# Kernel optimization log

Hardware: AMD Instinct MI355X
Metric: run time of the kernel (lower is better)

## Reference

```python
import jax, jax.numpy as jnp
import numpy as np

D = 128   # node feature dim
C = 2     # classes
N = 50000 # nodes
E = 500000  # edges (before self-loops)
H1 = 2    # conv1 heads
NEG_SLOPE = 0.2
BN_EPS = 1e-5


def setup_inputs() -> dict:
    key = jax.random.key(0)
    ks = jax.random.split(key, 24)
    rn = lambda k, shape, s=0.05: jax.random.normal(k, shape, dtype=jnp.float32) * s
    inp = {
        'x': jax.random.normal(ks[0], (N, D), dtype=jnp.float32),
        'edge_index': jax.random.randint(ks[1], (2, E), 0, N, dtype=jnp.int64),
        # conv1: GATConv(D, D, heads=2, concat=True)
        'W1': rn(ks[2], (D, H1 * D)),
        'att_src1': rn(ks[3], (H1, D)),
        'att_dst1': rn(ks[4], (H1, D)),
        'bias1': jnp.zeros((H1 * D,), jnp.float32),
        # conv2: GATConv(2D, D, heads=1, concat=False)
        'W2': rn(ks[5], (2 * D, D)),
        'att_src2': rn(ks[6], (1, D)),
        'att_dst2': rn(ks[7], (1, D)),
        'bias2': jnp.zeros((D,), jnp.float32),
        # lin1 = MLP([3D, 96]) : Linear -> ReLU -> BatchNorm1d
        'Wl': rn(ks[8], (3 * D, 96)), 'bl': jnp.zeros((96,), jnp.float32),
        'gl': jnp.ones((96,), jnp.float32), 'betal': jnp.zeros((96,), jnp.float32),
        # mlp1 = MLP([96, 96, C]) : two (Linear -> ReLU -> BN) blocks
        'Wa': rn(ks[9], (96, 96)), 'ba': jnp.zeros((96,), jnp.float32),
        'ga': jnp.ones((96,), jnp.float32), 'betaa': jnp.zeros((96,), jnp.float32),
        'Wb': rn(ks[10], (96, C)), 'bb': jnp.zeros((C,), jnp.float32),
        'gb': jnp.ones((C,), jnp.float32), 'betab': jnp.zeros((C,), jnp.float32),
    }
    return inp


def gat_conv(x, src, dst, W, att_src, att_dst, bias, heads, out_dim, concat):
    # PyG GATConv: h = x W -> [N,H,F]; per-edge logit leakyrelu(a_s.h_src + a_d.h_dst);
    # segment softmax over edges grouped by destination; weighted scatter-sum.
    n = x.shape[0]
    h = (x @ W).reshape(n, heads, out_dim)
    a_src = jnp.einsum('nhd,hd->nh', h, att_src)  # [N,H]
    a_dst = jnp.einsum('nhd,hd->nh', h, att_dst)
    alpha = jax.nn.leaky_relu(a_src[src] + a_dst[dst], NEG_SLOPE)  # [Etot,H]
    m = jax.ops.segment_max(alpha, dst, num_segments=n)            # [N,H]
    e = jnp.exp(alpha - m[dst])
    s = jax.ops.segment_sum(e, dst, num_segments=n)
    w = e / (s[dst] + 1e-16)                                       # [Etot,H]
    out = jax.ops.segment_sum(h[src] * w[:, :, None], dst, num_segments=n)  # [N,H,F]
    out = out.reshape(n, heads * out_dim) if concat else out.mean(axis=1)
    return out + bias


def mlp_block(x, W, b, gamma, beta):
    # Linear -> ReLU -> BatchNorm1d (training-mode batch stats, biased var)
    y = jax.nn.relu(x @ W + b)
    mu = y.mean(axis=0)
    var = ((y - mu) ** 2).mean(axis=0)
    return gamma * (y - mu) / jnp.sqrt(var + BN_EPS) + beta


def reference(x, edge_index, W1, att_src1, att_dst1, bias1,
              W2, att_src2, att_dst2, bias2,
              Wl, bl, gl, betal, Wa, ba, ga, betaa, Wb, bb, gb, betab):
    n = x.shape[0]
    # PyG GATConv default add_self_loops=True
    loops = jnp.arange(n, dtype=edge_index.dtype)
    src = jnp.concatenate([edge_index[0], loops])
    dst = jnp.concatenate([edge_index[1], loops])
    x1 = gat_conv(x, src, dst, W1, att_src1, att_dst1, bias1, H1, D, True)    # [N,2D]
    x2 = gat_conv(x1, src, dst, W2, att_src2, att_dst2, bias2, 1, D, False)   # [N,D]
    h = jnp.concatenate([x1, x2], axis=1)                                      # [N,3D]
    h = mlp_block(h, Wl, bl, gl, betal)     # lin1
    h = mlp_block(h, Wa, ba, ga, betaa)     # mlp1 layer 1
    h = mlp_block(h, Wb, bb, gb, betab)     # mlp1 layer 2
    return h
```

## Files before the change

kernel.cpp:

```cpp
#include <hip/hip_runtime.h>
#include <hip/hip_bf16.h>
#include <cstdint>
#include <cstddef>

#define NNODES 50000
#define NEDGES 500000
#define ETOT   (NEDGES + NNODES)

typedef __attribute__((ext_vector_type(8))) short short8;
typedef __attribute__((ext_vector_type(8))) unsigned short ushort8v;
typedef __attribute__((ext_vector_type(4))) float floatx4;
typedef __attribute__((ext_vector_type(4))) unsigned short ushort4v;

__device__ __forceinline__ unsigned short f2bf(float f) {
    union { __hip_bfloat16 h; unsigned short u; } cv;
    cv.h = __float2bfloat16(f);
    return cv.u;
}
__device__ __forceinline__ float bf2f(unsigned short u) {
    union { unsigned int i; float f; } cv;
    cv.i = ((unsigned int)u) << 16;
    return cv.f;
}

#define GBM 128
#define GBN 64
#define GBK 32

__global__ __launch_bounds__(256, 4) void gemm_mfma(
    const unsigned short* __restrict__ A, int lda,
    const unsigned short* __restrict__ Bt,
    float* __restrict__ C,
    unsigned short* __restrict__ Cb, int ldc,
    const float* __restrict__ bias,
    float* __restrict__ colsum, float* __restrict__ colsq,
    int M, int N, int K, int do_relu)
{
    __shared__ __attribute__((aligned(16))) unsigned short Alds[GBM * GBK];
    __shared__ __attribute__((aligned(16))) unsigned short Blds[GBN * GBK];
    __shared__ float scol[GBN], sqcol[GBN];

    int tid = threadIdx.x;
    int wave = tid >> 6, lane = tid & 63;
    int row0 = blockIdx.y * GBM;
    int col0 = blockIdx.x * GBN;
    int m = lane & 15, q = lane >> 4;

    floatx4 acc[2][4] = {};

    for (int k0 = 0; k0 < K; k0 += GBK) {
        #pragma unroll
        for (int i = 0; i < 2; ++i) {
            int c = tid + i * 256;
            int r = c >> 2, off = (c & 3) * 8;
            int gr = row0 + r;
            short8 v = {};
            if (gr < M) v = *(const short8*)(A + (size_t)gr * lda + k0 + off);
            *(short8*)(Alds + r * GBK + off) = v;
        }
        {
            int r = tid >> 2, off = (tid & 3) * 8;
            short8 v = *(const short8*)(Bt + (size_t)(col0 + r) * K + k0 + off);
            *(short8*)(Blds + r * GBK + off) = v;
        }
        __syncthreads();

        short8 a0 = *(const short8*)(Alds + (wave * 32 + m) * GBK + q * 8);
        short8 a1 = *(const short8*)(Alds + (wave * 32 + 16 + m) * GBK + q * 8);
        #pragma unroll
        for (int ct = 0; ct < 4; ++ct) {
            short8 b = *(const short8*)(Blds + (ct * 16 + m) * GBK + q * 8);
            acc[0][ct] = __builtin_amdgcn_mfma_f32_16x16x32_bf16(a0, b, acc[0][ct], 0, 0, 0);
            acc[1][ct] = __builtin_amdgcn_mfma_f32_16x16x32_bf16(a1, b, acc[1][ct], 0, 0, 0);
        }
        __syncthreads();
    }

    float ps[4] = {}, pq[4] = {};
    #pragma unroll
    for (int rt = 0; rt < 2; ++rt) {
        #pragma unroll
        for (int r = 0; r < 4; ++r) {
            int gr = row0 + wave * 32 + rt * 16 + q * 4 + r;
            #pragma unroll
            for (int ct = 0; ct < 4; ++ct) {
                int gc = col0 + ct * 16 + m;
                float v = acc[rt][ct][r];
                if (gc < N) {
                    float vb = v;
                    if (bias != nullptr) vb += bias[gc];
                    if (do_relu) vb = fmaxf(vb, 0.f);
                    if (gr < M) {
                        if (C  != nullptr) C[(size_t)gr * ldc + gc] = vb;
                        if (Cb != nullptr) Cb[(size_t)gr * ldc + gc] = f2bf(vb);
                        ps[ct] += vb; pq[ct] += vb * vb;
                    }
                }
            }
        }
    }
    if (colsum != nullptr) {
        if (tid < GBN) { scol[tid] = 0.f; sqcol[tid] = 0.f; }
        __syncthreads();
        #pragma unroll
        for (int ct = 0; ct < 4; ++ct) {
            atomicAdd(&scol[ct * 16 + m], ps[ct]);
            atomicAdd(&sqcol[ct * 16 + m], pq[ct]);
        }
        __syncthreads();
        if (tid < GBN) {
            int gc = col0 + tid;
            if (gc < N) {
                atomicAdd(&colsum[gc], scol[tid]);
                atomicAdd(&colsq[gc], sqcol[tid]);
            }
        }
    }
}

__global__ __launch_bounds__(256) void fold_cast(
    const float* __restrict__ W1, const float* __restrict__ as1v, const float* __restrict__ ad1v,
    const float* __restrict__ W2, const float* __restrict__ as2v, const float* __restrict__ ad2v,
    const float* __restrict__ Wl,
    float* __restrict__ U1, float* __restrict__ U2,
    unsigned short* __restrict__ W1t, unsigned short* __restrict__ W2t,
    unsigned short* __restrict__ Wlt)
{
    if (blockIdx.x < 64) {
        int g = threadIdx.x >> 5, l = threadIdx.x & 31;
        int task = blockIdx.x * 8 + g;
        float ss = 0.f, sd = 0.f;
        if (task < 256) {
            int d = task & 127, h = task >> 7;
            const float4 wv = *(const float4*)(W1 + d * 256 + h * 128 + l * 4);
            const float4 av = *(const float4*)(as1v + h * 128 + l * 4);
            const float4 bv = *(const float4*)(ad1v + h * 128 + l * 4);
            ss = wv.x * av.x + wv.y * av.y + wv.z * av.z + wv.w * av.w;
            sd = wv.x * bv.x + wv.y * bv.y + wv.z * bv.z + wv.w * bv.w;
        } else {
            int k = task - 256;
            const float4 wv = *(const float4*)(W2 + (size_t)k * 128 + l * 4);
            const float4 av = *(const float4*)(as2v + l * 4);
            const float4 bv = *(const float4*)(ad2v + l * 4);
            ss = wv.x * av.x + wv.y * av.y + wv.z * av.z + wv.w * av.w;
            sd = wv.x * bv.x + wv.y * bv.y + wv.z * bv.z + wv.w * bv.w;
        }
        #pragma unroll
        for (int off = 1; off < 32; off <<= 1) { ss += __shfl_xor(ss, off); sd += __shfl_xor(sd, off); }
        if (l == 0) {
            if (task < 256) {
                int d = task & 127, h = task >> 7;
                U1[h * 128 + d] = ss;
                U1[256 + h * 128 + d] = sd;
            } else {
                int k = task - 256;
                U2[k] = ss;
                U2[256 + k] = sd;
            }
        }
    } else {
        int i = (blockIdx.x - 64) * 256 + threadIdx.x;
        if (i < 32768) {
            int n = i >> 7, k = i & 127;
            W1t[i] = f2bf(W1[k * 256 + n]);
        } else if (i < 65536) {
            int j = i - 32768;
            int n = j >> 8, k = j & 255;
            W2t[j] = f2bf(W2[k * 128 + n]);
        } else if (i < 114688) {
            int j = i - 65536;
            int n = j / 384, k = j % 384;
            Wlt[j] = (n < 96) ? f2bf(Wl[(size_t)k * 96 + n]) : (unsigned short)0;
        }
    }
}

__global__ __launch_bounds__(256) void cast_x_att(
    const float* __restrict__ x, const float* __restrict__ U1,
    unsigned short* __restrict__ xb, float* __restrict__ as1, float* __restrict__ ad1)
{
    __shared__ float Us[512];
    int tid = threadIdx.x;
    Us[tid] = U1[tid];
    Us[tid + 256] = U1[tid + 256];
    __syncthreads();
    int g = tid >> 5, l = tid & 31;
    int n = blockIdx.x * 8 + g;
    if (n >= NNODES) return;
    const float4 v = *(const float4*)(x + (size_t)n * 128 + l * 4);
    ushort4v o;
    o.x = f2bf(v.x); o.y = f2bf(v.y); o.z = f2bf(v.z); o.w = f2bf(v.w);
    *(ushort4v*)(xb + (size_t)n * 128 + l * 4) = o;
    const float4 us0 = *(const float4*)(Us + l * 4);
    const float4 us1 = *(const float4*)(Us + 128 + l * 4);
    const float4 ud0 = *(const float4*)(Us + 256 + l * 4);
    const float4 ud1 = *(const float4*)(Us + 384 + l * 4);
    float s0 = v.x * us0.x + v.y * us0.y + v.z * us0.z + v.w * us0.w;
    float s1 = v.x * us1.x + v.y * us1.y + v.z * us1.z + v.w * us1.w;
    float d0 = v.x * ud0.x + v.y * ud0.y + v.z * ud0.z + v.w * ud0.w;
    float d1 = v.x * ud1.x + v.y * ud1.y + v.z * ud1.z + v.w * ud1.w;
    #pragma unroll
    for (int off = 1; off < 32; off <<= 1) {
        s0 += __shfl_xor(s0, off); s1 += __shfl_xor(s1, off);
        d0 += __shfl_xor(d0, off); d1 += __shfl_xor(d1, off);
    }
    if (l == 0) {
        as1[n * 2] = s0; as1[n * 2 + 1] = s1;
        ad1[n * 2] = d0; ad1[n * 2 + 1] = d1;
    }
}

__global__ void bnfold_a(const float* __restrict__ csum, const float* __restrict__ csq,
                         const float* __restrict__ gamma, const float* __restrict__ beta,
                         const float* __restrict__ Wa, const float* __restrict__ ba,
                         unsigned short* __restrict__ Wat2, float* __restrict__ ba_f) {
    __shared__ float scl[96], shf[96];
    int tid = threadIdx.x;
    if (tid < 96) {
        float mu  = csum[tid] / (float)NNODES;
        float var = csq[tid] / (float)NNODES - mu * mu;
        if (var < 0.f) var = 0.f;
        float sc = gamma[tid] * rsqrtf(var + 1e-5f);
        scl[tid] = sc; shf[tid] = beta[tid] - mu * sc;
    }
    __syncthreads();
    for (int idx = tid; idx < 128 * 96; idx += 256) {
        int n = idx / 96, k = idx % 96;
        Wat2[idx] = (n < 96) ? f2bf(scl[k] * Wa[k * 96 + n]) : (unsigned short)0;
    }
    if (tid < 96) {
        float s = ba[tid];
        for (int k = 0; k < 96; ++k) s += shf[k] * Wa[k * 96 + tid];
        ba_f[tid] = s;
    }
}

__global__ void bnfold_b(const float* __restrict__ csum, const float* __restrict__ csq,
                         const float* __restrict__ gamma, const float* __restrict__ beta,
                         const float* __restrict__ Wb, const float* __restrict__ bb,
                         unsigned short* __restrict__ Wbt, float* __restrict__ bb_f) {
    __shared__ float scl[96], shf[96];
    int tid = threadIdx.x;
    if (tid < 96) {
        float mu  = csum[tid] / (float)NNODES;
        float var = csq[tid] / (float)NNODES - mu * mu;
        if (var < 0.f) var = 0.f;
        float sc = gamma[tid] * rsqrtf(var + 1e-5f);
        scl[tid] = sc; shf[tid] = beta[tid] - mu * sc;
    }
    __syncthreads();
    for (int idx = tid; idx < 64 * 96; idx += 256) {
        int n = idx / 96, k = idx % 96;
        Wbt[idx] = (n < 2) ? f2bf(scl[k] * Wb[k * 2 + n]) : (unsigned short)0;
    }
    if (tid < 2) {
        float s = bb[tid];
        for (int k = 0; k < 96; ++k) s += shf[k] * Wb[k * 2 + tid];
        bb_f[tid] = s;
    }
}

__global__ void bn_fin_apply(const float* __restrict__ csum, const float* __restrict__ csq,
                             const float* __restrict__ gamma, const float* __restrict__ beta,
                             float* __restrict__ y, int total) {
    int i = blockIdx.x * blockDim.x + threadIdx.x;
    if (i >= total) return;
    int j = i & 1;
    float mu  = csum[j] / (float)NNODES;
    float var = csq[j] / (float)NNODES - mu * mu;
    if (var < 0.f) var = 0.f;
    float sc = gamma[j] * rsqrtf(var + 1e-5f);
    float sh = beta[j] - mu * sc;
    y[i] = y[i] * sc + sh;
}

__device__ __forceinline__ void edge_src_dst(const int* ei, int e, int& src, int& dst) {
    if (e < NEDGES) { src = ei[e]; dst = ei[NEDGES + e]; }
    else { src = e - NEDGES; dst = src; }
}

__global__ __launch_bounds__(256) void csr_count(const int* __restrict__ ei, int* __restrict__ cnt) {
    int e = blockIdx.x * blockDim.x + threadIdx.x;
    if (e >= ETOT) return;
    int src, dst; edge_src_dst(ei, e, src, dst); (void)src;
    atomicAdd(&cnt[dst], 1);
}

#define SCAN_CH 1024
#define SCAN_NB ((NNODES + SCAN_CH - 1) / SCAN_CH)

__global__ __launch_bounds__(256) void scan1(const int* __restrict__ cnt, int* __restrict__ part) {
    int t = threadIdx.x;
    int base = blockIdx.x * SCAN_CH + t * 4;
    int4 v = {0, 0, 0, 0};
    if (base + 3 < NNODES) v = *(const int4*)(cnt + base);
    else {
        if (base + 0 < NNODES) v.x = cnt[base + 0];
        if (base + 1 < NNODES) v.y = cnt[base + 1];
        if (base + 2 < NNODES) v.z = cnt[base + 2];
        if (base + 3 < NNODES) v.w = cnt[base + 3];
    }
    int s = v.x + v.y + v.z + v.w;
    __shared__ int sm[256];
    sm[t] = s;
    __syncthreads();
    for (int off = 128; off > 0; off >>= 1) {
        if (t < off) sm[t] += sm[t + off];
        __syncthreads();
    }
    if (t == 0) part[blockIdx.x] = sm[0];
}

__global__ __launch_bounds__(256) void scan23(const int* __restrict__ cnt, const int* __restrict__ part,
                                              int* __restrict__ rowstart, int* __restrict__ cursor) {
    __shared__ int sbase;
    int t = threadIdx.x;
    if (t < 64) {
        int v = (t < SCAN_NB) ? part[t] : 0;
        #pragma unroll
        for (int off = 1; off < 64; off <<= 1) {
            int u = __shfl_up(v, off);
            if (t >= off) v += u;
        }
        int ex = __shfl_up(v, 1);
        if (t == 0) ex = 0;
        if (t == (int)blockIdx.x) sbase = ex;
        if (blockIdx.x == 0 && t == 0) rowstart[NNODES] = ETOT;
    }
    int base = blockIdx.x * SCAN_CH + t * 4;
    int4 v = {0, 0, 0, 0};
    if (base + 3 < NNODES) v = *(const int4*)(cnt + base);
    else {
        if (base + 0 < NNODES) v.x = cnt[base + 0];
        if (base + 1 < NNODES) v.y = cnt[base + 1];
        if (base + 2 < NNODES) v.z = cnt[base + 2];
        if (base + 3 < NNODES) v.w = cnt[base + 3];
    }
    int s = v.x + v.y + v.z + v.w;
    __shared__ int sm[2][256];
    sm[0][t] = s;
    __syncthreads();
    int cur = 0;
    #pragma unroll
    for (int off = 1; off < 256; off <<= 1) {
        int nxt = cur ^ 1;
        int val = sm[cur][t];
        if (t >= off) val += sm[cur][t - off];
        sm[nxt][t] = val;
        __syncthreads();
        cur = nxt;
    }
    int p = sm[cur][t] - s + sbase;
    if (base + 0 < NNODES) { rowstart[base + 0] = p; cursor[base + 0] = p; } p += v.x;
    if (base + 1 < NNODES) { rowstart[base + 1] = p; cursor[base + 1] = p; } p += v.y;
    if (base + 2 < NNODES) { rowstart[base + 2] = p; cursor[base + 2] = p; } p += v.z;
    if (base + 3 < NNODES) { rowstart[base + 3] = p; cursor[base + 3] = p; }
}

__global__ __launch_bounds__(256) void csr_fill(const int* __restrict__ ei,
                                                int* __restrict__ cursor,
                                                int* __restrict__ esrc) {
    int e = blockIdx.x * blockDim.x + threadIdx.x;
    if (e >= ETOT) return;
    int src, dst; edge_src_dst(ei, e, src, dst);
    int pos = atomicAdd(&cursor[dst], 1);
    esrc[pos] = src;
}

__global__ __launch_bounds__(256, 4) void gat_conv1_fused(
    const int* __restrict__ rowstart, const int* __restrict__ esrc,
    const unsigned short* __restrict__ xb, const float* __restrict__ a_src,
    const float* __restrict__ a_dst, const unsigned short* __restrict__ W1t,
    const float* __restrict__ bias1, const float* __restrict__ U2,
    unsigned short* __restrict__ xcat, float* __restrict__ as2, float* __restrict__ ad2)
{
    __shared__ __attribute__((aligned(16))) unsigned short Alds[16 * 264];
    __shared__ float U2s[512];
    __shared__ float Bs[256];

    int tid = threadIdx.x;
    int t = tid & 15;
    int g = tid >> 4;
    int nb = blockIdx.x * 16;
    int n = nb + g;

    U2s[tid] = U2[tid];
    U2s[tid + 256] = U2[tid + 256];
    Bs[tid] = bias1[tid];

    int beg = rowstart[n], deg = rowstart[n + 1] - beg;
    const float2 adv = *(const float2*)(a_dst + (size_t)n * 2);
    float acc0[8] = {}, acc1[8] = {};

    if (deg <= 32) {
        int sa = 0, sb = 0;
        float la0 = -1e30f, la1 = -1e30f;
        float lb0 = -1e30f, lb1 = -1e30f;
        if (t < deg) {
            sa = esrc[beg + t];
            const float2 asv = *(const float2*)(a_src + (size_t)sa * 2);
            la0 = asv.x + adv.x; la0 = la0 >= 0.f ? la0 : 0.2f * la0;
            lb0 = asv.y + adv.y; lb0 = lb0 >= 0.f ? lb0 : 0.2f * lb0;
        }
        if (t + 16 < deg) {
            sb = esrc[beg + 16 + t];
            const float2 asv = *(const float2*)(a_src + (size_t)sb * 2);
            la1 = asv.x + adv.x; la1 = la1 >= 0.f ? la1 : 0.2f * la1;
            lb1 = asv.y + adv.y; lb1 = lb1 >= 0.f ? lb1 : 0.2f * lb1;
        }
        float m0 = fmaxf(la0, la1), m1 = fmaxf(lb0, lb1);
        #pragma unroll
        for (int off = 1; off < 16; off <<= 1) {
            m0 = fmaxf(m0, __shfl_xor(m0, off, 16));
            m1 = fmaxf(m1, __shfl_xor(m1, off, 16));
        }
        float ea0 = (t < deg)      ? __expf(la0 - m0) : 0.f;
        float ea1 = (t + 16 < deg) ? __expf(la1 - m0) : 0.f;
        float eb0 = (t < deg)      ? __expf(lb0 - m1) : 0.f;
        float eb1 = (t + 16 < deg) ? __expf(lb1 - m1) : 0.f;
        float s0 = ea0 + ea1, s1 = eb0 + eb1;
        #pragma unroll
        for (int off = 1; off < 16; off <<= 1) {
            s0 += __shfl_xor(s0, off, 16);
            s1 += __shfl_xor(s1, off, 16);
        }
        float i0 = 1.f / (s0 + 1e-16f), i1 = 1.f / (s1 + 1e-16f);
        float wa0 = ea0 * i0, wa1 = ea1 * i0;
        float wb0 = eb0 * i1, wb1 = eb1 * i1;

        int e = 0;
        for (; e + 3 < deg; e += 4) {
            int sx[4]; float w0x[4], w1x[4];
            #pragma unroll
            for (int u = 0; u < 4; ++u) {
                int ee = e + u;
                int hi = ee & 16, ln = ee & 15;
                sx[u]  = __shfl(hi ? sb  : sa,  ln, 16);
                w0x[u] = __shfl(hi ? wa1 : wa0, ln, 16);
                w1x[u] = __shfl(hi ? wb1 : wb0, ln, 16);
            }
            ushort8v hv[4];
            #pragma unroll
            for (int u = 0; u < 4; ++u)
                hv[u] = *(const ushort8v*)(xb + (size_t)sx[u] * 128 + t * 8);
            #pragma unroll
            for (int u = 0; u < 4; ++u) {
                #pragma unroll
                for (int j = 0; j < 8; ++j) {
                    float f = bf2f(hv[u][j]);
                    acc0[j] += w0x[u] * f;
                    acc1[j] += w1x[u] * f;
                }
            }
        }
        for (; e < deg; ++e) {
            int hi = e & 16, ln = e & 15;
            int   sX  = __shfl(hi ? sb  : sa,  ln, 16);
            float wX0 = __shfl(hi ? wa1 : wa0, ln, 16);
            float wX1 = __shfl(hi ? wb1 : wb0, ln, 16);
            const ushort8v hv = *(const ushort8v*)(xb + (size_t)sX * 128 + t * 8);
            #pragma unroll
            for (int j = 0; j < 8; ++j) {
                float f = bf2f(hv[j]);
                acc0[j] += wX0 * f; acc1[j] += wX1 * f;
            }
        }
    } else {
        float m0 = -1e30f, m1 = -1e30f;
        for (int idx = t; idx < deg; idx += 16) {
            int s = esrc[beg + idx];
            const float2 asv = *(const float2*)(a_src + (size_t)s * 2);
            float l0 = asv.x + adv.x; l0 = l0 >= 0.f ? l0 : 0.2f * l0;
            float l1 = asv.y + adv.y; l1 = l1 >= 0.f ? l1 : 0.2f * l1;
            m0 = fmaxf(m0, l0); m1 = fmaxf(m1, l1);
        }
        #pragma unroll
        for (int off = 1; off < 16; off <<= 1) {
            m0 = fmaxf(m0, __shfl_xor(m0, off, 16));
            m1 = fmaxf(m1, __shfl_xor(m1, off, 16));
        }
        float s0 = 0.f, s1 = 0.f;
        for (int idx = t; idx < deg; idx += 16) {
            int s = esrc[beg + idx];
            const float2 asv = *(const float2*)(a_src + (size_t)s * 2);
            float l0 = asv.x + adv.x; l0 = l0 >= 0.f ? l0 : 0.2f * l0;
            float l1 = asv.y + adv.y; l1 = l1 >= 0.f ? l1 : 0.2f * l1;
            s0 += __expf(l0 - m0); s1 += __expf(l1 - m1);
        }
        #pragma unroll
        for (int off = 1; off < 16; off <<= 1) {
            s0 += __shfl_xor(s0, off, 16);
            s1 += __shfl_xor(s1, off, 16);
        }
        float inv0 = 1.f / (s0 + 1e-16f), inv1 = 1.f / (s1 + 1e-16f);
        for (int e = 0; e < deg; ++e) {
            int s = esrc[beg + e];
            const float2 asv = *(const float2*)(a_src + (size_t)s * 2);
            float l0 = asv.x + adv.x; l0 = l0 >= 0.f ? l0 : 0.2f * l0;
            float l1 = asv.y + adv.y; l1 = l1 >= 0.f ? l1 : 0.2f * l1;
            float w0 = __expf(l0 - m0) * inv0, w1 = __expf(l1 - m1) * inv1;
            const ushort8v hv = *(const ushort8v*)(xb + (size_t)s * 128 + t * 8);
            #pragma unroll
            for (int j = 0; j < 8; ++j) {
                float f = bf2f(hv[j]);
                acc0[j] += w0 * f; acc1[j] += w1 * f;
            }
        }
    }

    {
        ushort8v o0, o1;
        #pragma unroll
        for (int j = 0; j < 8; ++j) { o0[j] = f2bf(acc0[j]); o1[j] = f2bf(acc1[j]); }
        *(ushort8v*)(Alds + g * 264 + t * 8) = o0;
        *(ushort8v*)(Alds + g * 264 + 128 + t * 8) = o1;
    }
    __syncthreads();

    int wave = tid >> 6, lane = tid & 63;
    int m = lane & 15, q = lane >> 4;
    int ncol0 = wave * 64;
    int kbase = (wave >= 2) ? 128 : 0;

    floatx4 cacc[4] = {};
    #pragma unroll
    for (int ks = 0; ks < 4; ++ks) {
        short8 a = *(const short8*)(Alds + m * 264 + kbase + ks * 32 + q * 8);
        #pragma unroll
        for (int ct = 0; ct < 4; ++ct) {
            short8 b = *(const short8*)(W1t + (size_t)(ncol0 + ct * 16 + m) * 128 + ks * 32 + q * 8);
            cacc[ct] = __builtin_amdgcn_mfma_f32_16x16x32_bf16(a, b, cacc[ct], 0, 0, 0);
        }
    }

    #pragma unroll
    for (int r = 0; r < 4; ++r) {
        int row = q * 4 + r;
        int gn = nb + row;
        float ds = 0.f, dd = 0.f;
        #pragma unroll
        for (int ct = 0; ct < 4; ++ct) {
            int col = ncol0 + ct * 16 + m;
            float vb = cacc[ct][r] + Bs[col];
            ds += vb * U2s[col];
            dd += vb * U2s[256 + col];
            xcat[(size_t)gn * 384 + col] = f2bf(vb);
        }
        #pragma unroll
        for (int off = 1; off < 16; off <<= 1) {
            ds += __shfl_xor(ds, off);
            dd += __shfl_xor(dd, off);
        }
        if (m == 0) {
            atomicAdd(&as2[gn], ds);
            atomicAdd(&ad2[gn], dd);
        }
    }
}

__global__ __launch_bounds__(256) void gat_gather_h1(
    const int* __restrict__ rowstart, const int* __restrict__ esrc,
    const unsigned short* __restrict__ hb, const float* __restrict__ a_src,
    const float* __restrict__ a_dst, const float* __restrict__ bias,
    unsigned short* __restrict__ xcat)
{
    int tid = threadIdx.x;
    int t = tid & 15;
    int g0 = (blockIdx.x * blockDim.x + tid) >> 4;
    int gstride = (gridDim.x * blockDim.x) >> 4;

    for (int n = g0; n < NNODES; n += gstride) {
        int beg = rowstart[n], deg = rowstart[n + 1] - beg;
        float ad0 = a_dst[n];
        float acc[8] = {};

        if (deg <= 32) {
            int sa = 0, sb = 0;
            float l0 = -1e30f, l1 = -1e30f;
            if (t < deg) {
                sa = esrc[beg + t];
                l0 = a_src[sa] + ad0; l0 = l0 >= 0.f ? l0 : 0.2f * l0;
            }
            if (t + 16 < deg) {
                sb = esrc[beg + 16 + t];
                l1 = a_src[sb] + ad0; l1 = l1 >= 0.f ? l1 : 0.2f * l1;
            }
            float m0 = fmaxf(l0, l1);
            #pragma unroll
            for (int off = 1; off < 16; off <<= 1)
                m0 = fmaxf(m0, __shfl_xor(m0, off, 16));
            float e0 = (t < deg)      ? __expf(l0 - m0) : 0.f;
            float e1 = (t + 16 < deg) ? __expf(l1 - m0) : 0.f;
            float s0 = e0 + e1;
            #pragma unroll
            for (int off = 1; off < 16; off <<= 1)
                s0 += __shfl_xor(s0, off, 16);
            float i0 = 1.f / (s0 + 1e-16f);
            float w0 = e0 * i0, w1 = e1 * i0;

            int e = 0;
            for (; e + 3 < deg; e += 4) {
                int sx[4]; float wx[4];
                #pragma unroll
                for (int u = 0; u < 4; ++u) {
                    int ee = e + u;
                    int hi = ee & 16, ln = ee & 15;
                    sx[u] = __shfl(hi ? sb : sa, ln, 16);
                    wx[u] = __shfl(hi ? w1 : w0, ln, 16);
                }
                ushort8v hv[4];
                #pragma unroll
                for (int u = 0; u < 4; ++u)
                    hv[u] = *(const ushort8v*)(hb + (size_t)sx[u] * 128 + t * 8);
                #pragma unroll
                for (int u = 0; u < 4; ++u) {
                    #pragma unroll
                    for (int j = 0; j < 8; ++j)
                        acc[j] += wx[u] * bf2f(hv[u][j]);
                }
            }
            for (; e < deg; ++e) {
                int hi = e & 16, ln = e & 15;
                int   sX = __shfl(hi ? sb : sa, ln, 16);
                float wX = __shfl(hi ? w1 : w0, ln, 16);
                const ushort8v hv = *(const ushort8v*)(hb + (size_t)sX * 128 + t * 8);
                #pragma unroll
                for (int j = 0; j < 8; ++j) acc[j] += wX * bf2f(hv[j]);
            }
        } else {
            float m0 = -1e30f;
            for (int idx = t; idx < deg; idx += 16) {
                int s = esrc[beg + idx];
                float l = a_src[s] + ad0; l = l >= 0.f ? l : 0.2f * l;
                m0 = fmaxf(m0, l);
            }
            #pragma unroll
            for (int off = 1; off < 16; off <<= 1)
                m0 = fmaxf(m0, __shfl_xor(m0, off, 16));
            float s0 = 0.f;
            for (int idx = t; idx < deg; idx += 16) {
                int s = esrc[beg + idx];
                float l = a_src[s] + ad0; l = l >= 0.f ? l : 0.2f * l;
                s0 += __expf(l - m0);
            }
            #pragma unroll
            for (int off = 1; off < 16; off <<= 1)
                s0 += __shfl_xor(s0, off, 16);
            float inv0 = 1.f / (s0 + 1e-16f);
            for (int e = 0; e < deg; ++e) {
                int s = esrc[beg + e];
                float l = a_src[s] + ad0; l = l >= 0.f ? l : 0.2f * l;
                float w = __expf(l - m0) * inv0;
                const ushort8v hv = *(const ushort8v*)(hb + (size_t)s * 128 + t * 8);
                #pragma unroll
                for (int j = 0; j < 8; ++j) acc[j] += w * bf2f(hv[j]);
            }
        }

        const float4 b0 = *(const float4*)(bias + t * 8);
        const float4 b1 = *(const float4*)(bias + t * 8 + 4);
        ushort8v o;
        o[0] = f2bf(acc[0] + b0.x); o[1] = f2bf(acc[1] + b0.y);
        o[2] = f2bf(acc[2] + b0.z); o[3] = f2bf(acc[3] + b0.w);
        o[4] = f2bf(acc[4] + b1.x); o[5] = f2bf(acc[5] + b1.y);
        o[6] = f2bf(acc[6] + b1.z); o[7] = f2bf(acc[7] + b1.w);
        *(ushort8v*)(xcat + (size_t)n * 384 + 256 + t * 8) = o;
    }
}

extern "C" void kernel_launch(void* const* d_in, const int* in_sizes, int n_in,
                              void* d_out, int out_size, void* d_ws, size_t ws_size,
                              hipStream_t stream) {
    const float* x        = (const float*)d_in[0];
    const int*   ei       = (const int*)d_in[1];
    const float* W1       = (const float*)d_in[2];
    const float* att_src1 = (const float*)d_in[3];
    const float* att_dst1 = (const float*)d_in[4];
    const float* bias1    = (const float*)d_in[5];
    const float* W2       = (const float*)d_in[6];
    const float* att_src2 = (const float*)d_in[7];
    const float* att_dst2 = (const float*)d_in[8];
    const float* bias2    = (const float*)d_in[9];
    const float* Wl       = (const float*)d_in[10];
    const float* bl       = (const float*)d_in[11];
    const float* gl       = (const float*)d_in[12];
    const float* betal    = (const float*)d_in[13];
    const float* Wa       = (const float*)d_in[14];
    const float* ba       = (const float*)d_in[15];
    const float* ga       = (const float*)d_in[16];
    const float* betaa    = (const float*)d_in[17];
    const float* Wb       = (const float*)d_in[18];
    const float* bb       = (const float*)d_in[19];
    const float* gb       = (const float*)d_in[20];
    const float* betab    = (const float*)d_in[21];
    float* out = (float*)d_out;
    char* ws = (char*)d_ws;

    const int N = NNODES;

    const size_t offY2b  = 0;
    const size_t offXcat = 19200000;
    const size_t offXb   = 57600000;
    const size_t offY1b  = 70400000;
    const size_t offW1t  = 105600000;
    const size_t offW2t  = 105665536;
    const size_t offWlt  = 105731072;
    const size_t offWat2 = 105829376;
    const size_t offWbt  = 105853952;
    const size_t offBaf  = 105866240;
    const size_t offBbf  = 105866640;
    const size_t offU1   = 105867264;
    const size_t offU2   = 105869312;
    const size_t offRow  = 106000000;
    const size_t offCur  = 106200128;
    const size_t offEsrc = 106400832;
    const size_t offPart = 108700000;
    const size_t offAs1  = 108800000;
    const size_t offAd1  = 109200000;
    const size_t offAs2  = 109600000;
    const size_t offAd2  = 109800000;
    const size_t offSt   = 110000000;

    unsigned short* y2b   = (unsigned short*)(ws + offY2b);
    unsigned short* xcat  = (unsigned short*)(ws + offXcat);
    unsigned short* xb    = (unsigned short*)(ws + offXb);
    unsigned short* hb2   = (unsigned short*)(ws + offXb);
    unsigned short* y1b   = (unsigned short*)(ws + offY1b);
    unsigned short* W1t   = (unsigned short*)(ws + offW1t);
    unsigned short* W2t   = (unsigned short*)(ws + offW2t);
    unsigned short* Wlt   = (unsigned short*)(ws + offWlt);
    unsigned short* Wat2  = (unsigned short*)(ws + offWat2);
    unsigned short* Wbt   = (unsigned short*)(ws + offWbt);
    float* ba_f = (float*)(ws + offBaf);
    float* bb_f = (float*)(ws + offBbf);
    float* U1   = (float*)(ws + offU1);
    float* U2   = (float*)(ws + offU2);
    int* rowst  = (int*)(ws + offRow);
    int* cursor = (int*)(ws + offCur);
    int* esrc   = (int*)(ws + offEsrc);
    int* part   = (int*)(ws + offPart);
    float* as1  = (float*)(ws + offAs1);
    float* ad1  = (float*)(ws + offAd1);
    float* as2  = (float*)(ws + offAs2);
    float* ad2  = (float*)(ws + offAd2);

    float* csum_l = (float*)(ws + offSt + 0);
    float* csq_l  = (float*)(ws + offSt + 512);
    float* csum_a = (float*)(ws + offSt + 2048);
    float* csq_a  = (float*)(ws + offSt + 2560);
    float* csum_b = (float*)(ws + offSt + 4096);
    float* csq_b  = (float*)(ws + offSt + 4608);

    hipMemsetAsync(ws + offRow, 0, (NNODES + 1) * sizeof(int), stream);
    hipMemsetAsync(ws + offAs1, 0, (offSt + 6144) - offAs1, stream);

    dim3 blk(256);
    int edgeBlocks = (ETOT + 255) / 256;
    int gatherBlocks = 2048;
    dim3 gemmRows((N + GBM - 1) / GBM);

    fold_cast<<<512, blk, 0, stream>>>(W1, att_src1, att_dst1, W2, att_src2, att_dst2,
                                       Wl, U1, U2, W1t, W2t, Wlt);
    cast_x_att<<<(N + 7) / 8, blk, 0, stream>>>(x, U1, xb, as1, ad1);

    csr_count<<<edgeBlocks, blk, 0, stream>>>(ei, rowst);
    scan1<<<SCAN_NB, blk, 0, stream>>>(rowst, part);
    scan23<<<SCAN_NB, blk, 0, stream>>>(rowst, part, rowst, cursor);
    csr_fill<<<edgeBlocks, blk, 0, stream>>>(ei, cursor, esrc);

    gat_conv1_fused<<<NNODES / 16, blk, 0, stream>>>(
        rowst, esrc, xb, as1, ad1, W1t, bias1, U2, xcat, as2, ad2);

    gemm_mfma<<<dim3(2, gemmRows.x), blk, 0, stream>>>(
        xcat, 384, W2t, nullptr, hb2, 128, nullptr, nullptr, nullptr,
        N, 128, 256, 0);
    gat_gather_h1<<<gatherBlocks, blk, 0, stream>>>(rowst, esrc, hb2, as2, ad2, bias2, xcat);

    gemm_mfma<<<dim3(2, gemmRows.x), blk, 0, stream>>>(
        xcat, 384, Wlt, nullptr, y1b, 96, bl, csum_l, csq_l,
        N, 96, 384, 1);
    bnfold_a<<<1, 256, 0, stream>>>(csum_l, csq_l, gl, betal, Wa, ba, Wat2, ba_f);

    gemm_mfma<<<dim3(2, gemmRows.x), blk, 0, stream>>>(
        y1b, 96, Wat2, nullptr, y2b, 96, ba_f, csum_a, csq_a,
        N, 96, 96, 1);
    bnfold_b<<<1, 256, 0, stream>>>(csum_a, csq_a, ga, betaa, Wb, bb, Wbt, bb_f);

    gemm_mfma<<<dim3(1, gemmRows.x), blk, 0, stream>>>(
        y2b, 96, Wbt, out, nullptr, 2, bb_f, csum_b, csq_b,
        N, 2, 96, 1);

    bn_fin_apply<<<(N * 2 + 255) / 256, blk, 0, stream>>>(csum_b, csq_b, gb, betab, out, N * 2);
}
```

Before: 349.1 us.

## Fuse conv2 linear projection into conv1 gather kernel via LDS-staged tile

The conv1 output tile is staged in shared memory instead of being written directly to global. It is then copied out to xcat with coalesced 16-byte stores and multiplied by W2 inside the same kernel, which removes the separate gemm_mfma launch and the re-read of xcat. hb2 moves to its own workspace region, and the launch bound's minimum blocks per CU rises from 4 to 8. The trade-off is extra syncs and more per-block work (eight k-steps with W2 loaded straight from global), plus register pressure from the higher occupancy target.

```diff
diff --git a/kernel.cpp b/kernel.cpp
--- a/kernel.cpp
+++ b/kernel.cpp
@@ -367,12 +367,14 @@
     esrc[pos] = src;
 }
 
-__global__ __launch_bounds__(256, 4) void gat_conv1_fused(
+__global__ __launch_bounds__(256, 8) void gat_conv12_fused(
     const int* __restrict__ rowstart, const int* __restrict__ esrc,
     const unsigned short* __restrict__ xb, const float* __restrict__ a_src,
     const float* __restrict__ a_dst, const unsigned short* __restrict__ W1t,
+    const unsigned short* __restrict__ W2t,
     const float* __restrict__ bias1, const float* __restrict__ U2,
-    unsigned short* __restrict__ xcat, float* __restrict__ as2, float* __restrict__ ad2)
+    unsigned short* __restrict__ xcat, unsigned short* __restrict__ hb2,
+    float* __restrict__ as2, float* __restrict__ ad2)
 {
     __shared__ __attribute__((aligned(16))) unsigned short Alds[16 * 264];
     __shared__ float U2s[512];
@@ -532,6 +534,7 @@
             cacc[ct] = __builtin_amdgcn_mfma_f32_16x16x32_bf16(a, b, cacc[ct], 0, 0, 0);
         }
     }
+    __syncthreads();
 
     #pragma unroll
     for (int r = 0; r < 4; ++r) {
@@ -544,7 +547,7 @@
             float vb = cacc[ct][r] + Bs[col];
             ds += vb * U2s[col];
             dd += vb * U2s[256 + col];
-            xcat[(size_t)gn * 384 + col] = f2bf(vb);
+            Alds[row * 264 + col] = f2bf(vb);
         }
         #pragma unroll
         for (int off = 1; off < 16; off <<= 1) {
@@ -554,6 +557,36 @@
         if (m == 0) {
             atomicAdd(&as2[gn], ds);
             atomicAdd(&ad2[gn], dd);
+        }
+    }
+    __syncthreads();
+
+    #pragma unroll
+    for (int c = tid; c < 512; c += 256) {
+        int row = c >> 5, ch = c & 31;
+        ushort8v v = *(const ushort8v*)(Alds + row * 264 + ch * 8);
+        *(ushort8v*)(xcat + (size_t)(nb + row) * 384 + ch * 8) = v;
+    }
+
+    floatx4 c2[2] = {};
+    #pragma unroll
+    for (int ks = 0; ks < 8; ++ks) {
+        short8 a = *(const short8*)(Alds + m * 264 + ks * 32 + q * 8);
+        #pragma unroll
+        for (int ct = 0; ct < 2; ++ct) {
+            int col = wave * 32 + ct * 16 + m;
+            short8 b = *(const short8*)(W2t + (size_t)col * 256 + ks * 32 + q * 8);
+            c2[ct] = __builtin_amdgcn_mfma_f32_16x16x32_bf16(a, b, c2[ct], 0, 0, 0);
+        }
+    }
+    #pragma unroll
+    for (int r = 0; r < 4; ++r) {
+        int row = q * 4 + r;
+        int gn = nb + row;
+        #pragma unroll
+        for (int ct = 0; ct < 2; ++ct) {
+            int col = wave * 32 + ct * 16 + m;
+            hb2[(size_t)gn * 128 + col] = f2bf(c2[ct][r]);
         }
     }
 }
@@ -702,6 +735,7 @@
     const size_t offXcat = 19200000;
     const size_t offXb   = 57600000;
     const size_t offY1b  = 70400000;
+    const size_t offHb2  = 80000000;
     const size_t offW1t  = 105600000;
     const size_t offW2t  = 105665536;
     const size_t offWlt  = 105731072;
@@ -724,8 +758,8 @@
     unsigned short* y2b   = (unsigned short*)(ws + offY2b);
     unsigned short* xcat  = (unsigned short*)(ws + offXcat);
     unsigned short* xb    = (unsigned short*)(ws + offXb);
-    unsigned short* hb2   = (unsigned short*)(ws + offXb);
     unsigned short* y1b   = (unsigned short*)(ws + offY1b);
+    unsigned short* hb2   = (unsigned short*)(ws + offHb2);
     unsigned short* W1t   = (unsigned short*)(ws + offW1t);
     unsigned short* W2t   = (unsigned short*)(ws + offW2t);
     unsigned short* Wlt   = (unsigned short*)(ws + offWlt);
@@ -768,12 +802,9 @@
     scan23<<<SCAN_NB, blk, 0, stream>>>(rowst, part, rowst, cursor);
     csr_fill<<<edgeBlocks, blk, 0, stream>>>(ei, cursor, esrc);
 
-    gat_conv1_fused<<<NNODES / 16, blk, 0, stream>>>(
-        rowst, esrc, xb, as1, ad1, W1t, bias1, U2, xcat, as2, ad2);
-
-    gemm_mfma<<<dim3(2, gemmRows.x), blk, 0, stream>>>(
-        xcat, 384, W2t, nullptr, hb2, 128, nullptr, nullptr, nullptr,
-        N, 128, 256, 0);
+    gat_conv12_fused<<<NNODES / 16, blk, 0, stream>>>(
+        rowst, esrc, xb, as1, ad1, W1t, W2t, bias1, U2, xcat, hb2, as2, ad2);
+
     gat_gather_h1<<<gatherBlocks, blk, 0, stream>>>(rowst, esrc, hb2, as2, ad2, bias2, xcat);
 
     gemm_mfma<<<dim3(2, gemmRows.x), blk, 0, stream>>>(
```

Result: slower. 364.0 us (+4.3%).
